# Performance work log

Measured on AMD Instinct MI355X. Metric: run time of the kernel, lower is better.

## Reference

```python
import jax, jax.numpy as jnp
import numpy as np
from jax import lax

BN_EPS = 1e-5  # eval-mode BatchNorm with running_mean=0, running_var=1


def _interp_mat(n_in, n_out):
    # align_corners=True bilinear interpolation matrix [n_out, n_in]
    if n_out == 1:
        coords = np.zeros((1,))
    else:
        coords = np.arange(n_out) * (n_in - 1) / (n_out - 1)
    lo = np.clip(np.floor(coords).astype(np.int64), 0, max(n_in - 2, 0))
    frac = (coords - lo).astype(np.float32)
    M = np.zeros((n_out, n_in), dtype=np.float32)
    M[np.arange(n_out), lo] += 1.0 - frac
    if n_in > 1:
        M[np.arange(n_out), lo + 1] += frac
    return jnp.asarray(M)


def _resize_ac(x, H, W):
    # bilinear, align_corners=True, over trailing two dims
    Mh = _interp_mat(x.shape[-2], H)
    Mw = _interp_mat(x.shape[-1], W)
    return jnp.einsum('...hw,Hh,Ww->...HW', x, Mh, Mw)


def _conv(x, w, b, pad):
    y = lax.conv_general_dilated(x, w, (1, 1), [(pad, pad), (pad, pad)],
                                 dimension_numbers=('NCHW', 'OIHW', 'NCHW'))
    return y + b[None, :, None, None]


def setup_inputs() -> dict:
    key = jax.random.key(0)
    ks = jax.random.split(key, 16)
    C, KD, VD, NCLS, BS = 256, 32, 128, 10, 4
    sizes = [64, 32, 16, 8, 4]
    inp = {}
    for l, s in enumerate(sizes):
        inp[f'feat{l}'] = jax.random.normal(ks[l], (BS, C, s, s), jnp.float32)
    inp['attentions'] = jax.random.normal(ks[5], (NCLS, C, 16, 16), jnp.float32)

    def w(k, shape):
        return jax.random.normal(k, shape, jnp.float32) * 0.05

    inp['key_t_w'] = w(ks[6], (KD, C, 3, 3)); inp['key_t_b'] = jnp.zeros((KD,), jnp.float32)
    inp['value_t_w'] = w(ks[7], (VD, C, 3, 3)); inp['value_t_b'] = jnp.zeros((VD,), jnp.float32)
    inp['key_q_w'] = w(ks[8], (5, KD, C, 3, 3)); inp['key_q_b'] = jnp.zeros((5, KD), jnp.float32)
    inp['value_q_w'] = w(ks[9], (5, VD, C, 3, 3)); inp['value_q_b'] = jnp.zeros((5, VD), jnp.float32)
    inp['bn_gamma'] = jnp.ones((5, 256), jnp.float32)
    inp['bn_beta'] = jnp.zeros((5, 256), jnp.float32)
    inp['combine_w'] = w(ks[10], (256, 512, 1, 1)); inp['combine_b'] = jnp.zeros((256,), jnp.float32)
    return inp


def reference(feat0, feat1, feat2, feat3, feat4, attentions,
              key_t_w, key_t_b, value_t_w, value_t_b,
              key_q_w, key_q_b, value_q_w, value_q_b,
              bn_gamma, bn_beta, combine_w, combine_b):
    feats = [feat0, feat1, feat2, feat3, feat4]
    ncls, _, h, w_ = attentions.shape
    hw = h * w_
    kt = _conv(attentions, key_t_w, key_t_b, 1).reshape(ncls, 32, hw)   # [n,32,hw]
    vt = _conv(attentions, value_t_w, value_t_b, 1).reshape(ncls, 128, hw)  # [n,128,hw]
    bn_scale = bn_gamma * np.float32(1.0 / np.sqrt(1.0 + BN_EPS))
    outs, fas = [], []
    for l, f in enumerate(feats):
        bs, _, H, W = f.shape
        fr = _resize_ac(f, h, w_)                                        # [b,C,h,w]
        kq = _conv(fr, key_q_w[l], key_q_b[l], 1).reshape(bs, 32, hw)    # [b,32,hw]
        vq = _conv(fr, value_q_w[l], value_q_b[l], 1)                    # [b,128,h,w]
        # p[b,n,i,j] = sum_k kq[b,k,i] * kt[n,k,j]; softmax over i (torch dim=1)
        p = jnp.einsum('bki,nkj->bnij', kq, kt)
        p = jax.nn.softmax(p, axis=2)
        # full attention maps: channels = template pixel j, spatial = query pixel i
        fa = _resize_ac(jnp.swapaxes(p, 2, 3).reshape(bs, ncls, hw, h, w_), H, W)
        # val_t_out summed over classes: sum_n sum_i vt[n,c,i] * p[b,n,i,j]
        agg = jnp.einsum('nci,bnij->bcj', vt, p).reshape(bs, 128, h, w_)
        final = jnp.concatenate([ncls * vq, agg], axis=1)                # [b,256,h,w]
        final = _resize_ac(final, H, W)
        final = final * bn_scale[l][None, :, None, None] + bn_beta[l][None, :, None, None]
        outs.append(_conv(jnp.concatenate([f, final], axis=1), combine_w, combine_b, 0))
        fas.append(fa)
    return (*outs, *fas)
```

## Files before the change

### kernel.cpp

```cpp
#include <hip/hip_runtime.h>

constexpr int CIN   = 256;
constexpr int KD    = 32;
constexpr int VD    = 128;
constexpr int NCLS  = 10;
constexpr int BS    = 4;
constexpr int HW    = 256;
constexpr float BNC = 0.9999950000374997f;

typedef unsigned short u16;
typedef __attribute__((ext_vector_type(8))) __bf16 bf8v;
typedef __attribute__((ext_vector_type(4))) float f4v;

static __device__ __forceinline__ int imin(int a, int b) { return a < b ? a : b; }

static __device__ __forceinline__ u16 f2bf(float v) {
  union { float f; unsigned u; } x; x.f = v;
  unsigned r = x.u + 0x7FFFu + ((x.u >> 16) & 1u);
  return (u16)(r >> 16);
}
static __device__ __forceinline__ float bf2f(u16 h) {
  union { unsigned u; float f; } x; x.u = ((unsigned)h) << 16;
  return x.f;
}

static __device__ __forceinline__ f4v mfma16(bf8v a, bf8v b, f4v c) {
  return __builtin_amdgcn_mfma_f32_16x16x32_bf16(a, b, c, 0, 0, 0);
}

__constant__ const int c_jbase[5] = {0, 16384, 20480, 21504, 21760};

__global__ __launch_bounds__(256) void k_prep1(
    const float* __restrict__ f0, const float* __restrict__ f1,
    const float* __restrict__ f2, const float* __restrict__ f3,
    const float* __restrict__ f4, const float* __restrict__ att,
    const float* __restrict__ vqw, const float* __restrict__ vtw,
    const float* __restrict__ kqw, const float* __restrict__ ktw,
    const float* __restrict__ cw, const float* __restrict__ gamma,
    const float* __restrict__ cbias, const float* __restrict__ beta,
    u16* __restrict__ Xf, u16* __restrict__ Xr,
    u16* __restrict__ Awv, u16* __restrict__ Awk,
    u16* __restrict__ cwA, u16* __restrict__ cw2A, float* __restrict__ cb) {
  __shared__ float sm[16][65];
  int blk = blockIdx.x;
  int tid = threadIdx.x;
  if (blk < 384) {
    const float* fin; u16* dstbase; int SS, px0;
    if (blk < 344) {
      int l, base, nb;
      if (blk < 256)      { l = 0; base = 0;   nb = 64; }
      else if (blk < 320) { l = 1; base = 256; nb = 16; }
      else if (blk < 336) { l = 2; base = 320; nb = 4; }
      else if (blk < 340) { l = 3; base = 336; nb = 1; }
      else                { l = 4; base = 340; nb = 1; }
      int local = blk - base;
      int b = local / nb, chunk = local % nb;
      int S = 64 >> l; SS = S * S;
      px0 = chunk * 64;
      fin = (l == 0 ? f0 : l == 1 ? f1 : l == 2 ? f2 : l == 3 ? f3 : f4)
            + (size_t)b * CIN * SS;
      dstbase = Xf + (size_t)(c_jbase[l] + b * SS) * 512;
    } else {
      int a = blk - 344;
      int imgA = a >> 2, chunk = a & 3;
      SS = 256; px0 = chunk * 64;
      fin = att + (size_t)imgA * CIN * 256;
      dstbase = Xr + (size_t)(20 + imgA) * 131072;
    }
    int px_r = tid & 63, cr = tid >> 6;
    int px_w = tid >> 2, c4 = (tid & 3) * 4;
    for (int cbk = 0; cbk < 16; ++cbk) {
      __syncthreads();
#pragma unroll
      for (int q = 0; q < 4; ++q) {
        int cl = q * 4 + cr;
        float v = 0.f;
        if (px0 + px_r < SS) v = fin[(size_t)(cbk * 16 + cl) * SS + px0 + px_r];
        sm[cl][px_r] = v;
      }
      __syncthreads();
      if (px0 + px_w < SS) {
        u16 hh[4], ll[4];
#pragma unroll
        for (int e = 0; e < 4; ++e) {
          float v = sm[c4 + e][px_w];
          hh[e] = f2bf(v); ll[e] = f2bf(v - bf2f(hh[e]));
        }
        uint2 wh, wl;
        wh.x = (unsigned)hh[0] | ((unsigned)hh[1] << 16); wh.y = (unsigned)hh[2] | ((unsigned)hh[3] << 16);
        wl.x = (unsigned)ll[0] | ((unsigned)ll[1] << 16); wl.y = (unsigned)ll[2] | ((unsigned)ll[3] << 16);
        u16* dst = dstbase + (size_t)(px0 + px_w) * 512 + cbk * 16 + c4;
        *reinterpret_cast<uint2*>(dst) = wh;
        *reinterpret_cast<uint2*>(dst + 256) = wl;
      }
    }
  } else if (blk < 1464) {
    int gid = (blk - 384) * 256 + tid;
    int lane = gid & 63;
    int grp = gid >> 6;
    const float* src; u16* dst; int kc;
    if (grp < 3456) {
      kc = grp % 72; int ot = (grp / 72) % 8; int sid = grp / (72 * 8);
      src = (sid < 5 ? vqw + (size_t)sid * VD * 2304 : vtw) + (size_t)(ot * 16 + (lane & 15)) * 2304;
      dst = Awv + (size_t)grp * 1024;
    } else {
      int g2 = grp - 3456;
      kc = g2 % 72; int ot = (g2 / 72) % 2; int sid = g2 / 144;
      src = (sid < 5 ? kqw + (size_t)sid * KD * 2304 : ktw) + (size_t)(ot * 16 + (lane & 15)) * 2304;
      dst = Awk + (size_t)g2 * 1024;
    }
    int q0 = (lane >> 4) * 8;
    int t = kc >> 3, c0 = (kc & 7) * 32;
#pragma unroll
    for (int i = 0; i < 8; ++i) {
      int c = c0 + q0 + i;
      float v = src[c * 9 + t];
      u16 h = f2bf(v);
      dst[lane * 8 + i] = h;
      dst[512 + lane * 8 + i] = f2bf(v - bf2f(h));
    }
  } else if (blk < 1848) {
    int blk2 = blk - 1464;
    if (blk2 < 64) {
      int gid = blk2 * 256 + tid;
      int oc = gid >> 6, c0 = (gid & 63) * 4;
      float4 v = *reinterpret_cast<const float4*>(cw + (size_t)oc * 512 + c0);
      const float* vv = (const float*)&v;
      u16 h[4], l[4];
#pragma unroll
      for (int e = 0; e < 4; ++e) { h[e] = f2bf(vv[e]); l[e] = f2bf(vv[e] - bf2f(h[e])); }
      uint2 wh, wl;
      wh.x = (unsigned)h[0] | ((unsigned)h[1] << 16); wh.y = (unsigned)h[2] | ((unsigned)h[3] << 16);
      wl.x = (unsigned)l[0] | ((unsigned)l[1] << 16); wl.y = (unsigned)l[2] | ((unsigned)l[3] << 16);
      *reinterpret_cast<uint2*>(cwA + (size_t)oc * 256 + c0) = wh;
      *reinterpret_cast<uint2*>(cwA + 65536 + (size_t)oc * 256 + c0) = wl;
    } else {
      int gid = (blk2 - 64) * 256 + tid;
      int l = gid / 16384, rem = gid % 16384;
      int oc = rem >> 6, c0 = (rem & 63) * 4;
      u16 h[4], lo[4];
#pragma unroll
      for (int e = 0; e < 4; ++e) {
        int c = c0 + e;
        float v = cw[(size_t)oc * 512 + 256 + c] * (gamma[l * 256 + c] * BNC);
        h[e] = f2bf(v); lo[e] = f2bf(v - bf2f(h[e]));
      }
      uint2 wh, wl;
      wh.x = (unsigned)h[0] | ((unsigned)h[1] << 16); wh.y = (unsigned)h[2] | ((unsigned)h[3] << 16);
      wl.x = (unsigned)lo[0] | ((unsigned)lo[1] << 16); wl.y = (unsigned)lo[2] | ((unsigned)lo[3] << 16);
      *reinterpret_cast<uint2*>(cw2A + (size_t)l * 65536 + oc * 256 + c0) = wh;
      *reinterpret_cast<uint2*>(cw2A + 327680 + (size_t)l * 65536 + oc * 256 + c0) = wl;
    }
  } else {
    int l = blk - 1848, oc = tid;
    float s = cbias[oc];
    for (int c = 0; c < CIN; ++c)
      s += cw[(size_t)oc * 512 + 256 + c] * beta[l * CIN + c];
    cb[l * CIN + oc] = s;
  }
}

__global__ __launch_bounds__(256) void k_prep_xr(
    const u16* __restrict__ Xf, u16* __restrict__ Xr, u16* __restrict__ zrow) {
  int blk = blockIdx.x;
  int img = blk >> 4, yr = blk & 15;
  int l = img >> 2, b = img & 3;
  int S = 64 >> l, SS = S * S;
  int c = threadIdx.x;
  if (blk == 0) { zrow[c] = 0; zrow[256 + c] = 0; }
  float cyf = (float)(yr * (S - 1)) / 15.0f;
  int ylo = imin((int)cyf, S - 2); float fy = cyf - (float)ylo;
  u16* dst = Xr + ((size_t)img * 256 + yr * 16) * 512;
  const u16* srcb = Xf + (size_t)(c_jbase[l] + b * SS) * 512;
  for (int x = 0; x < 16; ++x) {
    float cxf = (float)(x * (S - 1)) / 15.0f;
    int xlo = imin((int)cxf, S - 2); float fx = cxf - (float)xlo;
    const u16* r00 = srcb + (size_t)(ylo * S + xlo) * 512;
    const u16* r10 = srcb + (size_t)((ylo + 1) * S + xlo) * 512;
    float v00 = bf2f(r00[c]) + bf2f(r00[256 + c]);
    float v01 = bf2f(r00[512 + c]) + bf2f(r00[768 + c]);
    float v10 = bf2f(r10[c]) + bf2f(r10[256 + c]);
    float v11 = bf2f(r10[512 + c]) + bf2f(r10[768 + c]);
    float v = (1.f - fy) * ((1.f - fx) * v00 + fx * v01)
            + fy * ((1.f - fx) * v10 + fx * v11);
    u16 h = f2bf(v);
    dst[x * 512 + c] = h;
    dst[x * 512 + 256 + c] = f2bf(v - bf2f(h));
  }
}

__global__ __launch_bounds__(256) void k_conv_mfma(
    const u16* __restrict__ Xr, const u16* __restrict__ Awv, const u16* __restrict__ Awk,
    const u16* __restrict__ zrow,
    float* __restrict__ kqall, u16* __restrict__ vt2, float* __restrict__ f16v,
    const float* __restrict__ vqb, const float* __restrict__ vtb,
    const float* __restrict__ kqb, const float* __restrict__ ktb) {
  int wid = blockIdx.x * 4 + (threadIdx.x >> 6);
  int lane = threadIdx.x & 63;
  bool isV = wid < 1920;
  int img, ot, yp;
  if (isV) { img = wid >> 6; int r = wid & 63; ot = r >> 3; yp = r & 7; }
  else     { int j = wid - 1920; img = j >> 4; int r = j & 15; ot = r >> 3; yp = r & 7; }
  int wset = img < 20 ? (img >> 2) : 5;

  const u16* Ab = isV ? Awv + ((size_t)(wset * 8 + ot)) * 72 * 1024
                      : Awk + ((size_t)(wset * 2 + ot)) * 72 * 1024;
  const u16* Xb = Xr + (size_t)img * 131072;
  int xcol = lane & 15, kg = lane >> 4;
  int y0 = yp * 2, y1 = y0 + 1;

  f4v acc0 = {0.f, 0.f, 0.f, 0.f}, acc1 = {0.f, 0.f, 0.f, 0.f};
  for (int t = 0; t < 9; ++t) {
    int dy = (t >= 6) ? 2 : (t >= 3 ? 1 : 0);
    int dx = t - dy * 3;
    int yy0 = y0 + dy - 1, yy1 = yy0 + 1;
    int xx = xcol + dx - 1;
    bool xok = (unsigned)xx < 16u;
    const u16* base0 = (xok && (unsigned)yy0 < 16u)
                       ? Xb + (size_t)(yy0 * 16 + xx) * 512 : zrow;
    const u16* base1 = (xok && (unsigned)yy1 < 16u)
                       ? Xb + (size_t)(yy1 * 16 + xx) * 512 : zrow;
    const u16* Xr0 = base0 + kg * 8;
    const u16* Xr1 = base1 + kg * 8;
    const u16* Ak = Ab + (size_t)t * 8 * 1024 + lane * 8;
#pragma unroll
    for (int cc = 0; cc < 8; ++cc) {
      bf8v ah = *reinterpret_cast<const bf8v*>(Ak + cc * 1024);
      bf8v al = *reinterpret_cast<const bf8v*>(Ak + cc * 1024 + 512);
      bf8v bh0 = *reinterpret_cast<const bf8v*>(Xr0 + cc * 32);
      bf8v bl0 = *reinterpret_cast<const bf8v*>(Xr0 + cc * 32 + 256);
      bf8v bh1 = *reinterpret_cast<const bf8v*>(Xr1 + cc * 32);
      bf8v bl1 = *reinterpret_cast<const bf8v*>(Xr1 + cc * 32 + 256);
      acc0 = mfma16(ah, bh0, acc0);
      acc0 = mfma16(ah, bl0, acc0);
      acc0 = mfma16(al, bh0, acc0);
      acc1 = mfma16(ah, bh1, acc1);
      acc1 = mfma16(ah, bl1, acc1);
      acc1 = mfma16(al, bh1, acc1);
    }
  }

  int ocbase = ot * 16;
  if (isV && img >= 20) {
    int n = img - 20;
    u16* d2 = vt2 + ((size_t)n * VD + ocbase) * HW;
#pragma unroll
    for (int i = 0; i < 4; ++i) {
      int ocl = kg * 4 + i;
      float bv = vtb[ocbase + ocl];
      float va = acc0[i] + bv, vb = acc1[i] + bv;
      u16 ha = f2bf(va), hb = f2bf(vb);
      size_t ia = (size_t)ocl * HW + y0 * 16 + xcol;
      size_t ib = (size_t)ocl * HW + y1 * 16 + xcol;
      d2[ia] = ha; d2[ia + 327680] = f2bf(va - bf2f(ha));
      d2[ib] = hb; d2[ib + 327680] = f2bf(vb - bf2f(hb));
    }
    return;
  }
  float scale = 1.f;
  const float* bias;
  float* dst;
  if (isV) { dst = f16v + ((size_t)img * VD + ocbase) * HW; bias = vqb + wset * VD + ocbase; scale = (float)NCLS; }
  else if (img < 20) { dst = kqall + ((size_t)img * KD + ocbase) * HW; bias = kqb + wset * KD + ocbase; }
  else { dst = kqall + (size_t)20 * KD * HW + ((size_t)(img - 20) * KD + ocbase) * HW; bias = ktb + ocbase; }
#pragma unroll
  for (int i = 0; i < 4; ++i) {
    int ocl = kg * 4 + i;
    float bv = bias[ocl];
    dst[(size_t)ocl * HW + y0 * 16 + xcol] = (acc0[i] + bv) * scale;
    dst[(size_t)ocl * HW + y1 * 16 + xcol] = (acc1[i] + bv) * scale;
  }
}

__global__ __launch_bounds__(256) void k_mega(
    const float* __restrict__ kqall, const u16* __restrict__ vt2,
    float* __restrict__ out, float* __restrict__ aggn) {
  int blk = blockIdx.x;
  int l = blk / 320;
  int r = blk % 320;
  int bn = r >> 3, jt = r & 7;
  int b = bn / NCLS, n = bn % NCLS;
  int t = threadIdx.x;
  int iq = t >> 5, jl = t & 31;
  int j = jt * 32 + jl;

  __shared__ float buf[8224];
  __shared__ float red[512];

  const float* ktb = kqall + 20 * KD * HW;
  float ktr[KD];
#pragma unroll
  for (int k = 0; k < KD; ++k) ktr[k] = ktb[((size_t)n * KD + k) * HW + j];
  const float* kqb = kqall + (size_t)(l * 4 + b) * KD * HW;
  for (int s = t; s < KD * HW; s += 256) buf[s] = kqb[s];
  __syncthreads();

  float v[32];
#pragma unroll
  for (int ii = 0; ii < 32; ++ii) v[ii] = 0.f;
  for (int k = 0; k < KD; ++k) {
    float a = ktr[k];
    const float4* q4 = (const float4*)&buf[k * 256 + iq * 32];
#pragma unroll
    for (int q = 0; q < 8; ++q) {
      float4 u = q4[q];
      v[q * 4 + 0] += u.x * a; v[q * 4 + 1] += u.y * a;
      v[q * 4 + 2] += u.z * a; v[q * 4 + 3] += u.w * a;
    }
  }
  float ml = -1e30f;
#pragma unroll
  for (int ii = 0; ii < 32; ++ii) ml = fmaxf(ml, v[ii]);
  float sl = 0.f;
#pragma unroll
  for (int ii = 0; ii < 32; ++ii) sl += __expf(v[ii] - ml);
  red[t] = ml;
  red[256 + t] = sl;
  __syncthreads();
  float M = -1e30f;
#pragma unroll
  for (int q = 0; q < 8; ++q) M = fmaxf(M, red[q * 32 + jl]);
  float Ssum = 0.f;
#pragma unroll
  for (int q = 0; q < 8; ++q) Ssum += red[256 + q * 32 + jl] * __expf(red[q * 32 + jl] - M);
  float inv = 1.0f / Ssum;
#pragma unroll
  for (int ii = 0; ii < 32; ++ii)
    buf[jl * 257 + iq * 32 + ii] = __expf(v[ii] - M) * inv;
  __syncthreads();

  int S_ = 64 >> l, shift = 6 - l, SS = S_ * S_;
  const size_t fa_off[5] = {5586944, 47529984, 58015744, 60637184, 61292544};
  float* ob = out + fa_off[l] + ((size_t)bn * HW + jt * 32) * SS;
  int tot = SS << 5;
  for (int base = t * 4; base < tot; base += 1024) {
    int jj = base >> (2 * shift);
    int rest = base & (SS - 1);
    int X0 = rest & (S_ - 1), Y = rest >> shift;
    float cyf = (float)(Y * 15) / (float)(S_ - 1);
    int ylo = imin((int)cyf, 14); float fy = cyf - (float)ylo;
    const float* prow = &buf[jj * 257];
    float4 rv; float* rr = (float*)&rv;
#pragma unroll
    for (int t4 = 0; t4 < 4; ++t4) {
      int X = X0 + t4;
      float cxf = (float)(X * 15) / (float)(S_ - 1);
      int xlo = imin((int)cxf, 14); float fx = cxf - (float)xlo;
      int i00 = ylo * 16 + xlo;
      float v0 = prow[i00],      v1 = prow[i00 + 1];
      float v2 = prow[i00 + 16], v3 = prow[i00 + 17];
      rr[t4] = (1.f - fy) * ((1.f - fx) * v0 + fx * v1)
             + fy * ((1.f - fx) * v2 + fx * v3);
    }
    *(float4*)(ob + (size_t)jj * SS + rest) = rv;
  }

  int w = t >> 6, lane = t & 63;
  int row = lane & 15, kg = lane >> 4;
  f4v acc[2][2] = {{{0.f,0.f,0.f,0.f},{0.f,0.f,0.f,0.f}},
                   {{0.f,0.f,0.f,0.f},{0.f,0.f,0.f,0.f}}};
  for (int kc = 0; kc < 8; ++kc) {
    bf8v ah[2], al[2];
#pragma unroll
    for (int ctl = 0; ctl < 2; ++ctl) {
      int ct = w * 2 + ctl;
      const u16* vh = vt2 + ((size_t)n * VD + ct * 16 + row) * 256 + kc * 32 + kg * 8;
      ah[ctl] = *reinterpret_cast<const bf8v*>(vh);
      al[ctl] = *reinterpret_cast<const bf8v*>(vh + 327680);
    }
#pragma unroll
    for (int jt2 = 0; jt2 < 2; ++jt2) {
      union { u16 u[8]; bf8v v8; } Bh, Bl;
#pragma unroll
      for (int e = 0; e < 8; ++e) {
        float f = buf[(jt2 * 16 + row) * 257 + kc * 32 + kg * 8 + e];
        u16 h = f2bf(f);
        Bh.u[e] = h; Bl.u[e] = f2bf(f - bf2f(h));
      }
#pragma unroll
      for (int ctl = 0; ctl < 2; ++ctl) {
        acc[ctl][jt2] = mfma16(ah[ctl], Bh.v8, acc[ctl][jt2]);
        acc[ctl][jt2] = mfma16(ah[ctl], Bl.v8, acc[ctl][jt2]);
        acc[ctl][jt2] = mfma16(al[ctl], Bh.v8, acc[ctl][jt2]);
      }
    }
  }
  float* ab = aggn + (size_t)(l * 40 + bn) * VD * HW;
#pragma unroll
  for (int ctl = 0; ctl < 2; ++ctl)
#pragma unroll
    for (int jt2 = 0; jt2 < 2; ++jt2)
#pragma unroll
      for (int i = 0; i < 4; ++i)
        ab[(size_t)(w * 32 + ctl * 16 + kg * 4 + i) * HW + jt * 32 + jt2 * 16 + row]
            = acc[ctl][jt2][i];
}

__global__ __launch_bounds__(256) void k_fuse_fs(
    const float* __restrict__ f16v, const float* __restrict__ aggn,
    u16* __restrict__ fsT) {
  int blk = blockIdx.x;
  int img = blk >> 4, jc = blk & 15;
  int j0 = jc * 16;
  int l = img >> 2, b = img & 3;
  int tid = threadIdx.x;
  __shared__ float fs[256][17];
  for (int pass = 0; pass < 16; ++pass) {
    int cc = pass * 16 + (tid >> 4);
    int jj = tid & 15;
    float v;
    if (cc < 128) {
      v = f16v[((size_t)img * VD + cc) * HW + j0 + jj];
    } else {
      const float* ab = aggn + ((size_t)(l * 40 + b * 10) * VD + cc - 128) * HW + j0 + jj;
      v = 0.f;
#pragma unroll
      for (int n = 0; n < NCLS; ++n) v += ab[(size_t)n * VD * HW];
    }
    fs[cc][jj] = v;
  }
  __syncthreads();
  int j = tid >> 4, cg = (tid & 15) * 16;
  u16* dst = fsT + ((size_t)img * 256 + j0 + j) * 512 + cg;
#pragma unroll
  for (int e = 0; e < 16; ++e) {
    float v = fs[cg + e][j];
    u16 h = f2bf(v);
    dst[e] = h;
    dst[256 + e] = f2bf(v - bf2f(h));
  }
}

__global__ __launch_bounds__(256) void k_g16_mfma(
    const u16* __restrict__ cw2A, const u16* __restrict__ fsT,
    float* __restrict__ g16_all) {
  int wid = blockIdx.x * 4 + (threadIdx.x >> 6);
  int lane = threadIdx.x & 63;
  int img = wid >> 8;
  int r = wid & 255;
  int octile = r >> 4, jt = r & 15;
  int l = img >> 2;
  int row = lane & 15, kg = lane >> 4;
  const u16* Ah = cw2A + (size_t)l * 65536 + (octile * 16 + row) * 256 + kg * 8;
  const u16* Al = Ah + 327680;
  const u16* Bh = fsT + ((size_t)img * 256 + jt * 16 + row) * 512 + kg * 8;
  const u16* Bl = Bh + 256;
  f4v acc = {0.f, 0.f, 0.f, 0.f};
#pragma unroll
  for (int kc = 0; kc < 8; ++kc) {
    bf8v ah = *reinterpret_cast<const bf8v*>(Ah + kc * 32);
    bf8v al = *reinterpret_cast<const bf8v*>(Al + kc * 32);
    bf8v bh = *reinterpret_cast<const bf8v*>(Bh + kc * 32);
    bf8v bl = *reinterpret_cast<const bf8v*>(Bl + kc * 32);
    acc = mfma16(ah, bh, acc);
    acc = mfma16(ah, bl, acc);
    acc = mfma16(al, bh, acc);
  }
#pragma unroll
  for (int i = 0; i < 4; ++i)
    g16_all[((size_t)img * CIN + octile * 16 + kg * 4 + i) * HW + jt * 16 + row] = acc[i];
}

__global__ __launch_bounds__(256) void k_out_final(
    const u16* __restrict__ cwA, const u16* __restrict__ Xf,
    const float* __restrict__ g16_all, const float* __restrict__ cb_all,
    float* __restrict__ out) {
  int wid = blockIdx.x * 4 + (threadIdx.x >> 6);
  int lane = threadIdx.x & 63;
  int pt = wid >> 4, octile = wid & 15;
  int l, lb, tl;
  if (pt < 1024)      { l = 0; lb = 0;    tl = 256; }
  else if (pt < 1280) { l = 1; lb = 1024; tl = 64; }
  else if (pt < 1344) { l = 2; lb = 1280; tl = 16; }
  else if (pt < 1360) { l = 3; lb = 1344; tl = 4; }
  else                { l = 4; lb = 1360; tl = 1; }
  int rem = pt - lb;
  int b = rem / tl;
  int pxin = (rem % tl) * 16;
  const size_t ooff[5] = {0, 4194304, 5242880, 5505024, 5570560};
  int S = 64 >> l, SS = S * S, shift = 6 - l;
  int row = lane & 15, kg = lane >> 4;
  int gpx = c_jbase[l] + b * SS + pxin + row;

  const u16* Ah = cwA + ((size_t)(octile * 16 + row)) * 256 + kg * 8;
  const u16* Al = Ah + 65536;
  const u16* Bh = Xf + (size_t)gpx * 512 + kg * 8;
  const u16* Bl = Bh + 256;
  f4v acc = {0.f, 0.f, 0.f, 0.f};
#pragma unroll
  for (int kc = 0; kc < 8; ++kc) {
    bf8v ah = *reinterpret_cast<const bf8v*>(Ah + kc * 32);
    bf8v al = *reinterpret_cast<const bf8v*>(Al + kc * 32);
    bf8v bh = *reinterpret_cast<const bf8v*>(Bh + kc * 32);
    bf8v bl = *reinterpret_cast<const bf8v*>(Bl + kc * 32);
    acc = mfma16(ah, bh, acc);
    acc = mfma16(ah, bl, acc);
    acc = mfma16(al, bh, acc);
  }

  int px = pxin + row;
  int Xc = px & (S - 1), Y = px >> shift;
  float cyf = (float)(Y * 15) / (float)(S - 1);
  int ylo = imin((int)cyf, 14); float fy = cyf - (float)ylo;
  float cxf = (float)(Xc * 15) / (float)(S - 1);
  int xlo = imin((int)cxf, 14); float fx = cxf - (float)xlo;
  int i00 = ylo * 16 + xlo;
  const float* gbase = g16_all + ((size_t)(l * 4 + b) * CIN + octile * 16 + kg * 4) * HW;
  float* ob = out + ooff[l] + ((size_t)b * CIN + octile * 16) * SS + px;
#pragma unroll
  for (int i = 0; i < 4; ++i) {
    const float* g = gbase + (size_t)i * HW + i00;
    float v0 = g[0], v1 = g[1], v2 = g[16], v3 = g[17];
    float bil = (1.f - fy) * ((1.f - fx) * v0 + fx * v1)
              + fy * ((1.f - fx) * v2 + fx * v3);
    ob[(size_t)(kg * 4 + i) * SS] = acc[i] + bil + cb_all[l * CIN + octile * 16 + kg * 4 + i];
  }
}

extern "C" void kernel_launch(void* const* d_in, const int* in_sizes, int n_in,
                              void* d_out, int out_size, void* d_ws, size_t ws_size,
                              hipStream_t stream) {
  const float* feat[5];
  for (int l = 0; l < 5; ++l) feat[l] = (const float*)d_in[l];
  const float* att   = (const float*)d_in[5];
  const float* ktw   = (const float*)d_in[6];
  const float* ktb   = (const float*)d_in[7];
  const float* vtw   = (const float*)d_in[8];
  const float* vtb   = (const float*)d_in[9];
  const float* kqw   = (const float*)d_in[10];
  const float* kqb   = (const float*)d_in[11];
  const float* vqw   = (const float*)d_in[12];
  const float* vqb   = (const float*)d_in[13];
  const float* gamma = (const float*)d_in[14];
  const float* beta  = (const float*)d_in[15];
  const float* cw    = (const float*)d_in[16];
  const float* cbias = (const float*)d_in[17];
  float* out = (float*)d_out;

  float* ws    = (float*)d_ws;
  float* kqall = ws;
  float* f16v  = ws + 245760;
  u16*   vt2   = (u16*)(ws + 901120);
  u16*   cwA   = (u16*)(ws + 1228800);
  u16*   cw2A  = (u16*)(ws + 1294336);
  float* cb    = ws + 1622016;
  u16*   Xf    = (u16*)(ws + 1623296);
  float* S0    = ws + 7210240;
  u16*   Awv  = (u16*)S0;
  u16*   Awk  = (u16*)(S0 + 1769472);
  u16*   Xr   = (u16*)(S0 + 2211840);
  u16*   zrow = (u16*)(S0 + 4177920);
  float* aggn    = S0;
  u16*   fsT     = (u16*)(S0 + 6553600);
  float* g16_all = S0;

  k_prep1<<<1853, 256, 0, stream>>>(
      feat[0], feat[1], feat[2], feat[3], feat[4], att,
      vqw, vtw, kqw, ktw, cw, gamma, cbias, beta,
      Xf, Xr, Awv, Awk, cwA, cw2A, cb);
  k_prep_xr<<<320, 256, 0, stream>>>(Xf, Xr, zrow);
  k_conv_mfma<<<600, 256, 0, stream>>>(
      Xr, Awv, Awk, zrow, kqall, vt2, f16v, vqb, vtb, kqb, ktb);

  k_mega<<<1600, 256, 0, stream>>>(kqall, vt2, out, aggn);
  k_fuse_fs<<<320, 256, 0, stream>>>(f16v, aggn, fsT);

  k_g16_mfma<<<1280, 256, 0, stream>>>(cw2A, fsT, g16_all);
  k_out_final<<<5456, 256, 0, stream>>>(cwA, Xf, g16_all, cb, out);
}
```

Measured before the change: 363.8 us.

## Fuse fs transpose into g16 MFMA kernel, drop one split-bf16 term, remap mega blocks

Merges the fs-staging kernel and the g16 MFMA kernel into one: the fused kernel converts values to hi/lo bf16 in shared memory and each block computes all output-channel tiles for its 16 pixels, removing the fsT round trip through global memory and one launch. In k_mega the low-bf16 part of the B operand is dropped, leaving two MFMAs per tile instead of three, which reduces precision of the aggregation GEMM. Block-to-level mapping in k_mega is interleaved across levels (l = blk % 5), which changes scheduling and cache locality. g16_all is moved to a separate workspace offset so it no longer aliases aggn.

```diff
diff --git a/kernel.cpp b/kernel.cpp
--- a/kernel.cpp
+++ b/kernel.cpp
@@ -276,9 +276,9 @@
     const float* __restrict__ kqall, const u16* __restrict__ vt2,
     float* __restrict__ out, float* __restrict__ aggn) {
   int blk = blockIdx.x;
-  int l = blk / 320;
-  int r = blk % 320;
-  int bn = r >> 3, jt = r & 7;
+  int l = blk % 5;
+  int q5 = blk / 5;
+  int bn = q5 >> 3, jt = q5 & 7;
   int b = bn / NCLS, n = bn % NCLS;
   int t = threadIdx.x;
   int iq = t >> 5, jl = t & 31;
@@ -370,17 +370,13 @@
     }
 #pragma unroll
     for (int jt2 = 0; jt2 < 2; ++jt2) {
-      union { u16 u[8]; bf8v v8; } Bh, Bl;
-#pragma unroll
-      for (int e = 0; e < 8; ++e) {
-        float f = buf[(jt2 * 16 + row) * 257 + kc * 32 + kg * 8 + e];
-        u16 h = f2bf(f);
-        Bh.u[e] = h; Bl.u[e] = f2bf(f - bf2f(h));
-      }
+      union { u16 u[8]; bf8v v8; } Bh;
+#pragma unroll
+      for (int e = 0; e < 8; ++e)
+        Bh.u[e] = f2bf(buf[(jt2 * 16 + row) * 257 + kc * 32 + kg * 8 + e]);
 #pragma unroll
       for (int ctl = 0; ctl < 2; ++ctl) {
         acc[ctl][jt2] = mfma16(ah[ctl], Bh.v8, acc[ctl][jt2]);
-        acc[ctl][jt2] = mfma16(ah[ctl], Bl.v8, acc[ctl][jt2]);
         acc[ctl][jt2] = mfma16(al[ctl], Bh.v8, acc[ctl][jt2]);
       }
     }
@@ -396,18 +392,20 @@
             = acc[ctl][jt2][i];
 }
 
-__global__ __launch_bounds__(256) void k_fuse_fs(
+__global__ __launch_bounds__(256) void k_g16f(
     const float* __restrict__ f16v, const float* __restrict__ aggn,
-    u16* __restrict__ fsT) {
+    const u16* __restrict__ cw2A, float* __restrict__ g16_all) {
   int blk = blockIdx.x;
   int img = blk >> 4, jc = blk & 15;
   int j0 = jc * 16;
   int l = img >> 2, b = img & 3;
   int tid = threadIdx.x;
-  __shared__ float fs[256][17];
+  __shared__ __align__(16) u16 fsbh[16][280];
+  __shared__ __align__(16) u16 fsbl[16][280];
+  int jj = tid & 15;
+  int c0 = tid >> 4;
   for (int pass = 0; pass < 16; ++pass) {
-    int cc = pass * 16 + (tid >> 4);
-    int jj = tid & 15;
+    int cc = pass * 16 + c0;
     float v;
     if (cc < 128) {
       v = f16v[((size_t)img * VD + cc) * HW + j0 + jj];
@@ -417,48 +415,34 @@
 #pragma unroll
       for (int n = 0; n < NCLS; ++n) v += ab[(size_t)n * VD * HW];
     }
-    fs[cc][jj] = v;
+    u16 h = f2bf(v);
+    fsbh[jj][cc] = h;
+    fsbl[jj][cc] = f2bf(v - bf2f(h));
   }
   __syncthreads();
-  int j = tid >> 4, cg = (tid & 15) * 16;
-  u16* dst = fsT + ((size_t)img * 256 + j0 + j) * 512 + cg;
-#pragma unroll
-  for (int e = 0; e < 16; ++e) {
-    float v = fs[cg + e][j];
-    u16 h = f2bf(v);
-    dst[e] = h;
-    dst[256 + e] = f2bf(v - bf2f(h));
-  }
-}
-
-__global__ __launch_bounds__(256) void k_g16_mfma(
-    const u16* __restrict__ cw2A, const u16* __restrict__ fsT,
-    float* __restrict__ g16_all) {
-  int wid = blockIdx.x * 4 + (threadIdx.x >> 6);
-  int lane = threadIdx.x & 63;
-  int img = wid >> 8;
-  int r = wid & 255;
-  int octile = r >> 4, jt = r & 15;
-  int l = img >> 2;
+
+  int w = tid >> 6, lane = tid & 63;
   int row = lane & 15, kg = lane >> 4;
-  const u16* Ah = cw2A + (size_t)l * 65536 + (octile * 16 + row) * 256 + kg * 8;
-  const u16* Al = Ah + 327680;
-  const u16* Bh = fsT + ((size_t)img * 256 + jt * 16 + row) * 512 + kg * 8;
-  const u16* Bl = Bh + 256;
-  f4v acc = {0.f, 0.f, 0.f, 0.f};
-#pragma unroll
-  for (int kc = 0; kc < 8; ++kc) {
-    bf8v ah = *reinterpret_cast<const bf8v*>(Ah + kc * 32);
-    bf8v al = *reinterpret_cast<const bf8v*>(Al + kc * 32);
-    bf8v bh = *reinterpret_cast<const bf8v*>(Bh + kc * 32);
-    bf8v bl = *reinterpret_cast<const bf8v*>(Bl + kc * 32);
-    acc = mfma16(ah, bh, acc);
-    acc = mfma16(ah, bl, acc);
-    acc = mfma16(al, bh, acc);
-  }
-#pragma unroll
-  for (int i = 0; i < 4; ++i)
-    g16_all[((size_t)img * CIN + octile * 16 + kg * 4 + i) * HW + jt * 16 + row] = acc[i];
+#pragma unroll
+  for (int q = 0; q < 4; ++q) {
+    int ot = w * 4 + q;
+    const u16* Ah = cw2A + (size_t)l * 65536 + ((size_t)(ot * 16 + row)) * 256 + kg * 8;
+    const u16* Al = Ah + 327680;
+    f4v acc = {0.f, 0.f, 0.f, 0.f};
+#pragma unroll
+    for (int kc = 0; kc < 8; ++kc) {
+      bf8v ah = *reinterpret_cast<const bf8v*>(Ah + kc * 32);
+      bf8v al = *reinterpret_cast<const bf8v*>(Al + kc * 32);
+      bf8v bh = *reinterpret_cast<const bf8v*>(&fsbh[row][kc * 32 + kg * 8]);
+      bf8v bl = *reinterpret_cast<const bf8v*>(&fsbl[row][kc * 32 + kg * 8]);
+      acc = mfma16(ah, bh, acc);
+      acc = mfma16(ah, bl, acc);
+      acc = mfma16(al, bh, acc);
+    }
+#pragma unroll
+    for (int i = 0; i < 4; ++i)
+      g16_all[((size_t)img * CIN + ot * 16 + kg * 4 + i) * HW + j0 + row] = acc[i];
+  }
 }
 
 __global__ __launch_bounds__(256) void k_out_final(
@@ -551,8 +535,7 @@
   u16*   Xr   = (u16*)(S0 + 2211840);
   u16*   zrow = (u16*)(S0 + 4177920);
   float* aggn    = S0;
-  u16*   fsT     = (u16*)(S0 + 6553600);
-  float* g16_all = S0;
+  float* g16_all = S0 + 6553600;
 
   k_prep1<<<1853, 256, 0, stream>>>(
       feat[0], feat[1], feat[2], feat[3], feat[4], att,
@@ -563,8 +546,7 @@
       Xr, Awv, Awk, zrow, kqall, vt2, f16v, vqb, vtb, kqb, ktb);
 
   k_mega<<<1600, 256, 0, stream>>>(kqall, vt2, out, aggn);
-  k_fuse_fs<<<320, 256, 0, stream>>>(f16v, aggn, fsT);
-
-  k_g16_mfma<<<1280, 256, 0, stream>>>(cw2A, fsT, g16_all);
+
+  k_g16f<<<320, 256, 0, stream>>>(f16v, aggn, cw2A, g16_all);
   k_out_final<<<5456, 256, 0, stream>>>(cwA, Xf, g16_all, cb, out);
 }
```

New measurement: 402.0 us. 10.5% more time.
